# Performance work log

Hardware: AMD Instinct MI355X
Metric: run time of the kernel (lower is better)

The kernel has to match this reference:

```python
import jax, jax.numpy as jnp
import numpy as np

N_HEADS = 16
EPS = 1e-4


def setup_inputs() -> dict:
    key = jax.random.key(0)
    ks = jax.random.split(key, 9)
    B, L, E = 4, 4096, 1024
    s = 1.0 / np.sqrt(E)
    return {
        "x": jax.random.normal(ks[0], (B, L, E), dtype=jnp.float32),
        "Wq": jax.random.normal(ks[1], (E, E), dtype=jnp.float32) * s,
        "bq": jax.random.normal(ks[2], (E,), dtype=jnp.float32) * 0.01,
        "Wk": jax.random.normal(ks[3], (E, E), dtype=jnp.float32) * s,
        "bk": jax.random.normal(ks[4], (E,), dtype=jnp.float32) * 0.01,
        "Wv": jax.random.normal(ks[5], (E, E), dtype=jnp.float32) * s,
        "bv": jax.random.normal(ks[6], (E,), dtype=jnp.float32) * 0.01,
        "Wo": jax.random.normal(ks[7], (E, E), dtype=jnp.float32) * s,
        "bo": jax.random.normal(ks[8], (E,), dtype=jnp.float32) * 0.01,
    }


def _cosformer(x, Wq, bq, Wk, bk, Wv, bv, Wo, bo):
    B, L, E = x.shape
    H = N_HEADS
    hd = E // H
    # torch Linear: y = x @ W.T + b; self-attention so q=k=v source is x
    q = jax.nn.relu(jnp.einsum('ble,fe->blf', x, Wq) + bq)
    k = jax.nn.relu(jnp.einsum('ble,fe->blf', x, Wk) + bk)
    v = jnp.einsum('ble,fe->blf', x, Wv) + bv
    # (B, L, E) -> (B*H, L, hd)  [matches torch view(L, B*H, hd).transpose(0,1)]
    def split_heads(t):
        return t.reshape(B, L, H, hd).transpose(0, 2, 1, 3).reshape(B * H, L, hd)
    q, k, v = split_heads(q), split_heads(k), split_heads(v)
    m = L  # src_len == tgt_len
    idx = (np.pi / 2) * jnp.arange(1, m + 1, dtype=jnp.float32) / m  # (m,)
    sin = jnp.sin(idx)[None, :, None]
    cos = jnp.cos(idx)[None, :, None]
    q_ = jnp.concatenate([q * sin, q * cos], axis=-1)  # (BH, L, 2hd)
    k_ = jnp.concatenate([k * sin, k * cos], axis=-1)
    kv = jnp.einsum('nld,nlm->ndm', k_, v)             # (BH, 2hd, hd)
    z = 1.0 / jnp.maximum(jnp.einsum('nld,nd->nl', q_, k_.sum(axis=1)), EPS)
    attn = jnp.einsum('nld,ndm->nlm', q_, kv) * z[:, :, None]  # (BH, L, hd)
    # (B*H, L, hd) -> (B, L, E)
    out = attn.reshape(B, H, L, hd).transpose(0, 2, 1, 3).reshape(B, L, E)
    return jnp.einsum('ble,fe->blf', out, Wo) + bo


def reference(x, Wq, bq, Wk, bk, Wv, bv, Wo, bo):
    return _cosformer(x, Wq, bq, Wk, bk, Wv, bv, Wo, bo)
```

## Files before the change

kernel.cpp:

```cpp
#include <hip/hip_runtime.h>


typedef unsigned short u16;
typedef unsigned int u32;
typedef __attribute__((ext_vector_type(8))) __bf16 bf16x8;
typedef __attribute__((ext_vector_type(4))) float f32x4;

#define PI_HALF 1.57079632679489662f
#define EPS_Z 1e-4f

__device__ __forceinline__ u16 f32_to_bf16(float f) {
    union { float f; unsigned int u; } x; x.f = f;
    unsigned int lsb = (x.u >> 16) & 1u;
    x.u += 0x7fffu + lsb;
    return (u16)(x.u >> 16);
}
__device__ __forceinline__ float bf16_to_f32(u16 u) {
    union { float f; unsigned int u; } x; x.u = ((unsigned int)u) << 16;
    return x.f;
}

typedef __attribute__((address_space(1))) void amdgpu_global_t;
typedef __attribute__((address_space(3))) void amdgpu_lds_t;
__device__ __forceinline__ void async_load16(const u16* g, u16* l) {
    __builtin_amdgcn_global_load_lds((amdgpu_global_t*)g, (amdgpu_lds_t*)l, 16, 0, 0);
}

__global__ __launch_bounds__(256) void cvt_bf16(const float* __restrict__ in,
                                                u16* __restrict__ out, int n4) {
    int i = blockIdx.x * 256 + threadIdx.x;
    if (i >= n4) return;
    float4 f = ((const float4*)in)[i];
    ushort4 o;
    o.x = f32_to_bf16(f.x); o.y = f32_to_bf16(f.y);
    o.z = f32_to_bf16(f.z); o.w = f32_to_bf16(f.w);
    ((ushort4*)out)[i] = o;
}

__global__ __launch_bounds__(256) void cvt_w4(const float* __restrict__ w0,
                                              const float* __restrict__ w1,
                                              const float* __restrict__ w2,
                                              const float* __restrict__ w3,
                                              u16* __restrict__ wcat) {
    const float* src = (blockIdx.y == 0) ? w0 : (blockIdx.y == 1) ? w1
                     : (blockIdx.y == 2) ? w2 : w3;
    u16* dst = wcat + (size_t)blockIdx.y * 1048576;
    int i = blockIdx.x * 256 + threadIdx.x;
    float4 f = ((const float4*)src)[i];
    ushort4 o;
    o.x = f32_to_bf16(f.x); o.y = f32_to_bf16(f.y);
    o.z = f32_to_bf16(f.z); o.w = f32_to_bf16(f.w);
    ((ushort4*)dst)[i] = o;
}

__global__ __launch_bounds__(256) void gemm_qkv(const u16* __restrict__ A,
                                                const u16* __restrict__ Wcat,
                                                const float* __restrict__ bq,
                                                const float* __restrict__ bk,
                                                const float* __restrict__ bv,
                                                u16* __restrict__ qo,
                                                u16* __restrict__ kTo,
                                                u16* __restrict__ vTo) {
    __shared__ u16 As[128 * 32];
    __shared__ u16 Bs[128 * 32];
    const int K = 1024;
    const int tid  = threadIdx.x;
    const int wave = tid >> 6;
    const int lane = tid & 63;
    const int quad = lane >> 4;
    const int l15  = lane & 15;
    const long tileM = (long)blockIdx.x * 128;
    const long tileN = (long)blockIdx.y * 128;
    const int mat = blockIdx.y >> 3;
    const float* bias = (mat == 0) ? bq : (mat == 1) ? bk : bv;
    const int wm = (wave >> 1) * 64;
    const int wn = (wave & 1) * 64;
    const int s_row = wave * 32 + (lane >> 2);
    const int s_col = (lane & 3) * 8;

    const u16* gA = A    + (tileM + s_row) * (long)K + s_col;
    const u16* gB = Wcat + (tileN + s_row) * (long)K + s_col;
    u16* lA = &As[wave * 1024];
    u16* lB = &Bs[wave * 1024];

    f32x4 acc[4][4] = {};

    for (int kb = 0; kb < K; kb += 32) {
        async_load16(gA,                lA);
        async_load16(gA + 16 * (long)K, lA + 512);
        async_load16(gB,                lB);
        async_load16(gB + 16 * (long)K, lB + 512);
        gA += 32; gB += 32;
        __syncthreads();
        bf16x8 af[4], bf[4];
#pragma unroll
        for (int i = 0; i < 4; i++) {
            af[i] = *(const bf16x8*)&As[(wm + i * 16 + l15) * 32 + quad * 8];
            bf[i] = *(const bf16x8*)&Bs[(wn + i * 16 + l15) * 32 + quad * 8];
        }
#pragma unroll
        for (int i = 0; i < 4; i++)
#pragma unroll
            for (int j = 0; j < 4; j++)
                acc[i][j] = __builtin_amdgcn_mfma_f32_16x16x32_bf16(
                    af[i], bf[j], acc[i][j], 0, 0, 0);
        __syncthreads();
    }

    if (mat == 0) {
#pragma unroll
        for (int j = 0; j < 4; j++) {
            const int nl = (int)(tileN + wn + j * 16 + l15) & 1023;
            const float bv_ = bias[nl];
#pragma unroll
            for (int i = 0; i < 4; i++) {
                const long m0 = tileM + wm + i * 16 + quad * 4;
#pragma unroll
                for (int r = 0; r < 4; r++) {
                    float v = fmaxf(acc[i][j][r] + bv_, 0.0f);
                    qo[(m0 + r) * 1024 + nl] = f32_to_bf16(v);
                }
            }
        }
    } else {
        u16* outT = (mat == 1) ? kTo : vTo;
        const bool relu = (mat == 1);
#pragma unroll
        for (int j = 0; j < 4; j++) {
            const int nl = (int)(tileN + wn + j * 16 + l15) & 1023;
            const float bv_ = bias[nl];
#pragma unroll
            for (int i = 0; i < 4; i++) {
                const long m0 = tileM + wm + i * 16 + quad * 4;
                float v0 = acc[i][j][0] + bv_;
                float v1 = acc[i][j][1] + bv_;
                float v2 = acc[i][j][2] + bv_;
                float v3 = acc[i][j][3] + bv_;
                if (relu) {
                    v0 = fmaxf(v0, 0.0f); v1 = fmaxf(v1, 0.0f);
                    v2 = fmaxf(v2, 0.0f); v3 = fmaxf(v3, 0.0f);
                }
                u32 p0 = (u32)f32_to_bf16(v0) | ((u32)f32_to_bf16(v1) << 16);
                u32 p1 = (u32)f32_to_bf16(v2) | ((u32)f32_to_bf16(v3) << 16);
                u32* dst = (u32*)(outT + (size_t)nl * 16384 + m0);
                dst[0] = p0; dst[1] = p1;
            }
        }
    }
}

__global__ __launch_bounds__(256) void gemm_o(const u16* __restrict__ A,
                                              const u16* __restrict__ Bw,
                                              const float* __restrict__ bias,
                                              float* __restrict__ Cout,
                                              int M, int N, int K) {
    __shared__ u16 As[128 * 32];
    __shared__ u16 Bs[128 * 32];
    const int tid  = threadIdx.x;
    const int wave = tid >> 6;
    const int lane = tid & 63;
    const int quad = lane >> 4;
    const int l15  = lane & 15;
    const long tileM = (long)blockIdx.x * 128;
    const long tileN = (long)blockIdx.y * 128;
    const int wm = (wave >> 1) * 64;
    const int wn = (wave & 1) * 64;
    const int s_row = wave * 32 + (lane >> 2);
    const int s_col = (lane & 3) * 8;

    const u16* gA = A  + (tileM + s_row) * (long)K + s_col;
    const u16* gB = Bw + (tileN + s_row) * (long)K + s_col;
    u16* lA = &As[wave * 1024];
    u16* lB = &Bs[wave * 1024];

    f32x4 acc[4][4] = {};

    for (int kb = 0; kb < K; kb += 32) {
        async_load16(gA,                lA);
        async_load16(gA + 16 * (long)K, lA + 512);
        async_load16(gB,                lB);
        async_load16(gB + 16 * (long)K, lB + 512);
        gA += 32; gB += 32;
        __syncthreads();
        bf16x8 af[4], bf[4];
#pragma unroll
        for (int i = 0; i < 4; i++) {
            af[i] = *(const bf16x8*)&As[(wm + i * 16 + l15) * 32 + quad * 8];
            bf[i] = *(const bf16x8*)&Bs[(wn + i * 16 + l15) * 32 + quad * 8];
        }
#pragma unroll
        for (int i = 0; i < 4; i++)
#pragma unroll
            for (int j = 0; j < 4; j++)
                acc[i][j] = __builtin_amdgcn_mfma_f32_16x16x32_bf16(
                    af[i], bf[j], acc[i][j], 0, 0, 0);
        __syncthreads();
    }

#pragma unroll
    for (int j = 0; j < 4; j++) {
        const long n = tileN + wn + j * 16 + l15;
        const float bv = bias[n];
#pragma unroll
        for (int i = 0; i < 4; i++) {
            const long m0 = tileM + wm + i * 16 + quad * 4;
#pragma unroll
            for (int r = 0; r < 4; r++)
                Cout[(m0 + r) * (long)N + n] = acc[i][j][r] + bv;
        }
    }
}

__global__ __launch_bounds__(256) void kv_mfma(const u16* __restrict__ kT,
                                               const u16* __restrict__ vT,
                                               u16* __restrict__ part) {
    const int tid = threadIdx.x;
    const int wave = tid >> 6, lane = tid & 63;
    const int quad = lane >> 4, l15 = lane & 15;
    const int head = blockIdx.y;
    const int b = head >> 4, h = head & 15;
    const long col0 = (long)b * 4096 + blockIdx.x * 256 + quad * 8;
    const bool use_cos = (wave >> 1) != 0;
    const int mbase = wave * 32;

    const u16* ka[2];
#pragma unroll
    for (int i = 0; i < 2; i++) {
        const int d = (mbase + i * 16 + l15) & 63;
        ka[i] = kT + (size_t)(h * 64 + d) * 16384 + col0;
    }
    const u16* va[4];
#pragma unroll
    for (int j = 0; j < 4; j++) {
        const int n = j * 16 + l15;
        va[j] = vT + (size_t)(h * 64 + n) * 16384 + col0;
    }

    float sv[8], cv[8];
#pragma unroll
    for (int e = 0; e < 8; e++) {
        float ang = (PI_HALF / 4096.0f) * (float)(blockIdx.x * 256 + quad * 8 + e + 1);
        sv[e] = sinf(ang); cv[e] = cosf(ang);
    }
    const float cD = 0.9999247018391445f;
    const float sD = 0.0122715382857199f;

    bf16x8 onesf;
#pragma unroll
    for (int e = 0; e < 8; e++)
        onesf[e] = (l15 == 0) ? (__bf16)1.0f : (__bf16)0.0f;

    f32x4 acc[2][5] = {};

    for (int kt = 0; kt < 8; kt++) {
        bf16x8 kraw[2], bfr[5];
#pragma unroll
        for (int i = 0; i < 2; i++) kraw[i] = *(const bf16x8*)(ka[i] + kt * 32);
#pragma unroll
        for (int j = 0; j < 4; j++) bfr[j] = *(const bf16x8*)(va[j] + kt * 32);
        bfr[4] = onesf;
        bf16x8 af[2];
#pragma unroll
        for (int i = 0; i < 2; i++)
#pragma unroll
            for (int e = 0; e < 8; e++)
                af[i][e] = (__bf16)((float)kraw[i][e] * (use_cos ? cv[e] : sv[e]));
#pragma unroll
        for (int i = 0; i < 2; i++)
#pragma unroll
            for (int j = 0; j < 5; j++)
                acc[i][j] = __builtin_amdgcn_mfma_f32_16x16x32_bf16(
                    af[i], bfr[j], acc[i][j], 0, 0, 0);
#pragma unroll
        for (int e = 0; e < 8; e++) {
            const float ns = sv[e] * cD + cv[e] * sD;
            cv[e] = cv[e] * cD - sv[e] * sD;
            sv[e] = ns;
        }
    }

    u16* op = part + ((size_t)blockIdx.x * 64 + head) * 10240;
#pragma unroll
    for (int i = 0; i < 2; i++)
#pragma unroll
        for (int j = 0; j < 5; j++)
#pragma unroll
            for (int r = 0; r < 4; r++)
                op[(mbase + i * 16 + quad * 4 + r) * 80 + j * 16 + l15] =
                    f32_to_bf16(acc[i][j][r]);
}

__global__ __launch_bounds__(256) void kv_reduce_t(const u16* __restrict__ part,
                                                   u16* __restrict__ Bt) {
    __shared__ float accs[32 * 81];
    const int head = blockIdx.y, d2t = blockIdx.x;
    const u16* bp = part + (size_t)head * 10240 + d2t * 32 * 80;
    for (int idx = threadIdx.x; idx < 2560; idx += 256) {
        float s = 0.0f;
#pragma unroll
        for (int c = 0; c < 16; c++)
            s += bf16_to_f32(bp[(size_t)c * 655360 + idx]);
        const int d2 = idx / 80, n = idx - d2 * 80;
        accs[d2 * 81 + n] = s;
    }
    __syncthreads();
    for (int idx = threadIdx.x; idx < 2560; idx += 256) {
        const int n = idx >> 5, d2 = idx & 31;
        Bt[(size_t)head * 10240 + n * 128 + d2t * 32 + d2] =
            f32_to_bf16(accs[d2 * 81 + n]);
    }
}

__global__ __launch_bounds__(256) void attn_mfma(const u16* __restrict__ qb,
                                                 const u16* __restrict__ Bt,
                                                 u16* __restrict__ merged) {
    __shared__ __align__(16) u16 As[128 * 72];
    __shared__ __align__(16) u16 Bs[80 * 136];
    const int tid = threadIdx.x;
    const int wave = tid >> 6, lane = tid & 63;
    const int quad = lane >> 4, l15 = lane & 15;
    const int head = blockIdx.y;
    const int b = head >> 4, h = head & 15;
    const int tm = blockIdx.x * 128;
    const long b4 = (long)b * 4096;

    for (int c = tid; c < 1024; c += 256) {
        const int row = c >> 3, c8 = c & 7;
        uint4 t = *(const uint4*)(qb + (b4 + tm + row) * 1024 + h * 64 + c8 * 8);
        *(uint4*)&As[row * 72 + c8 * 8] = t;
    }
    for (int c = tid; c < 1280; c += 256) {
        const int row = c >> 4, c16 = c & 15;
        uint4 t = *(const uint4*)(Bt + (long)head * 10240 + row * 128 + c16 * 8);
        *(uint4*)&Bs[row * 136 + c16 * 8] = t;
    }
    const int wm = wave * 32;
    float snl[2], csl[2];
#pragma unroll
    for (int i = 0; i < 2; i++) {
        const int l = tm + wm + i * 16 + l15;
        const float idx = PI_HALF * (float)(l + 1) * (1.0f / 4096.0f);
        snl[i] = sinf(idx); csl[i] = cosf(idx);
    }
    __syncthreads();

    f32x4 acc[2][5] = {};
#pragma unroll
    for (int kb = 0; kb < 4; kb++) {
        const int qc = (kb & 1) * 32 + quad * 8;
        bf16x8 af[2];
#pragma unroll
        for (int i = 0; i < 2; i++) {
            bf16x8 raw = *(const bf16x8*)&As[(wm + i * 16 + l15) * 72 + qc];
            const float s = (kb < 2) ? snl[i] : csl[i];
            bf16x8 sc;
#pragma unroll
            for (int e = 0; e < 8; e++) sc[e] = (__bf16)((float)raw[e] * s);
            af[i] = sc;
        }
        bf16x8 bf[5];
#pragma unroll
        for (int j = 0; j < 5; j++)
            bf[j] = *(const bf16x8*)&Bs[(j * 16 + l15) * 136 + kb * 32 + quad * 8];
#pragma unroll
        for (int i = 0; i < 2; i++)
#pragma unroll
            for (int j = 0; j < 5; j++)
                acc[i][j] = __builtin_amdgcn_mfma_f32_16x16x32_bf16(
                    af[i], bf[j], acc[i][j], 0, 0, 0);
    }

#pragma unroll
    for (int i = 0; i < 2; i++) {
        float z[4];
#pragma unroll
        for (int r = 0; r < 4; r++) {
            const float den = __shfl(acc[i][4][r], lane & 0x30, 64);
            z[r] = 1.0f / fmaxf(den, EPS_Z);
        }
#pragma unroll
        for (int j = 0; j < 4; j++)
#pragma unroll
            for (int r = 0; r < 4; r++) {
                const int l = tm + wm + i * 16 + quad * 4 + r;
                merged[(b4 + l) * 1024 + h * 64 + j * 16 + l15] =
                    f32_to_bf16(acc[i][j][r] * z[r]);
            }
    }
}

extern "C" void kernel_launch(void* const* d_in, const int* in_sizes, int n_in,
                              void* d_out, int out_size, void* d_ws, size_t ws_size,
                              hipStream_t stream) {
    (void)in_sizes; (void)n_in; (void)out_size; (void)ws_size;
    const float* x  = (const float*)d_in[0];
    const float* Wq = (const float*)d_in[1];
    const float* bq = (const float*)d_in[2];
    const float* Wk = (const float*)d_in[3];
    const float* bk = (const float*)d_in[4];
    const float* Wv = (const float*)d_in[5];
    const float* bv = (const float*)d_in[6];
    const float* Wo = (const float*)d_in[7];
    const float* bo = (const float*)d_in[8];
    float* out = (float*)d_out;

    const int M = 16384, E = 1024;
    char* ws = (char*)d_ws;
    const size_t MB = 1048576;
    u16* xb   = (u16*)(ws);
    u16* qb   = (u16*)(ws + 32 * MB);
    u16* kTb  = (u16*)(ws + 64 * MB);
    u16* vTb  = (u16*)(ws + 96 * MB);
    u16* wcat = (u16*)(ws + 128 * MB);
    u16* wob  = wcat + 3 * (size_t)E * E;
    u16* Btb  = (u16*)(ws + 136 * MB);
    u16* partb = xb;
    u16* mergedb = kTb;

    cvt_bf16<<<dim3(M * E / 4 / 256), dim3(256), 0, stream>>>(x, xb, M * E / 4);
    cvt_w4<<<dim3(E * E / 4 / 256, 4), dim3(256), 0, stream>>>(Wq, Wk, Wv, Wo, wcat);

    gemm_qkv<<<dim3(M / 128, 24), dim3(256), 0, stream>>>(xb, wcat, bq, bk, bv,
                                                          qb, kTb, vTb);

    kv_mfma<<<dim3(16, 64), dim3(256), 0, stream>>>(kTb, vTb, partb);
    kv_reduce_t<<<dim3(4, 64), dim3(256), 0, stream>>>(partb, Btb);
    attn_mfma<<<dim3(32, 64), dim3(256), 0, stream>>>(qb, Btb, mergedb);

    gemm_o<<<dim3(M / 128, E / 128), dim3(256), 0, stream>>>(mergedb, wob, bo,
                                                             out, M, E, E);
}
```

Before: 413.5 us.

## Move K/V transpose out of QKV GEMM epilogue; load attention operands directly

The QKV GEMM now writes K and V row-major like Q, with one shared epilogue, instead of scattering transposed 4-byte stores. Two new LDS-tiled transpose kernels then build the K^T and V^T layouts that kv_mfma expects. Workspace buffers are re-aliased so the transposes can reuse freed regions. Separately, attn_mfma drops its LDS staging and barrier and loads Q and the per-head KV matrix straight from global memory into registers. The cost is an extra read and write of K and V plus two more kernel launches.

```diff
diff --git a/kernel.cpp b/kernel.cpp
--- a/kernel.cpp
+++ b/kernel.cpp
@@ -59,8 +59,8 @@
                                                 const float* __restrict__ bk,
                                                 const float* __restrict__ bv,
                                                 u16* __restrict__ qo,
-                                                u16* __restrict__ kTo,
-                                                u16* __restrict__ vTo) {
+                                                u16* __restrict__ ko,
+                                                u16* __restrict__ vo) {
     __shared__ u16 As[128 * 32];
     __shared__ u16 Bs[128 * 32];
     const int K = 1024;
@@ -73,6 +73,8 @@
     const long tileN = (long)blockIdx.y * 128;
     const int mat = blockIdx.y >> 3;
     const float* bias = (mat == 0) ? bq : (mat == 1) ? bk : bv;
+    u16* outp = (mat == 0) ? qo : (mat == 1) ? ko : vo;
+    const bool relu = (mat < 2);
     const int wm = (wave >> 1) * 64;
     const int wn = (wave & 1) * 64;
     const int s_row = wave * 32 + (lane >> 2);
@@ -107,43 +109,18 @@
         __syncthreads();
     }
 
-    if (mat == 0) {
-#pragma unroll
-        for (int j = 0; j < 4; j++) {
-            const int nl = (int)(tileN + wn + j * 16 + l15) & 1023;
-            const float bv_ = bias[nl];
-#pragma unroll
-            for (int i = 0; i < 4; i++) {
-                const long m0 = tileM + wm + i * 16 + quad * 4;
-#pragma unroll
-                for (int r = 0; r < 4; r++) {
-                    float v = fmaxf(acc[i][j][r] + bv_, 0.0f);
-                    qo[(m0 + r) * 1024 + nl] = f32_to_bf16(v);
-                }
-            }
-        }
-    } else {
-        u16* outT = (mat == 1) ? kTo : vTo;
-        const bool relu = (mat == 1);
-#pragma unroll
-        for (int j = 0; j < 4; j++) {
-            const int nl = (int)(tileN + wn + j * 16 + l15) & 1023;
-            const float bv_ = bias[nl];
-#pragma unroll
-            for (int i = 0; i < 4; i++) {
-                const long m0 = tileM + wm + i * 16 + quad * 4;
-                float v0 = acc[i][j][0] + bv_;
-                float v1 = acc[i][j][1] + bv_;
-                float v2 = acc[i][j][2] + bv_;
-                float v3 = acc[i][j][3] + bv_;
-                if (relu) {
-                    v0 = fmaxf(v0, 0.0f); v1 = fmaxf(v1, 0.0f);
-                    v2 = fmaxf(v2, 0.0f); v3 = fmaxf(v3, 0.0f);
-                }
-                u32 p0 = (u32)f32_to_bf16(v0) | ((u32)f32_to_bf16(v1) << 16);
-                u32 p1 = (u32)f32_to_bf16(v2) | ((u32)f32_to_bf16(v3) << 16);
-                u32* dst = (u32*)(outT + (size_t)nl * 16384 + m0);
-                dst[0] = p0; dst[1] = p1;
+#pragma unroll
+    for (int j = 0; j < 4; j++) {
+        const int nl = (int)(tileN + wn + j * 16 + l15) & 1023;
+        const float bv_ = bias[nl];
+#pragma unroll
+        for (int i = 0; i < 4; i++) {
+            const long m0 = tileM + wm + i * 16 + quad * 4;
+#pragma unroll
+            for (int r = 0; r < 4; r++) {
+                float v = acc[i][j][r] + bv_;
+                if (relu) v = fmaxf(v, 0.0f);
+                outp[(m0 + r) * 1024 + nl] = f32_to_bf16(v);
             }
         }
     }
@@ -211,6 +188,33 @@
     }
 }
 
+__global__ __launch_bounds__(256) void transpose_64(const u16* __restrict__ src,
+                                                    u16* __restrict__ dst) {
+    __shared__ u32 tl[64 * 33];
+    const int t = threadIdx.x;
+    const int tok0 = blockIdx.x * 64;
+    const int f0 = blockIdx.y * 64;
+    const int lp = t >> 3;
+    const int d0 = (t & 7) * 8;
+    const u16* s0 = src + (size_t)(tok0 + 2 * lp) * 1024 + f0 + d0;
+    uint4 r0 = *(const uint4*)s0;
+    uint4 r1 = *(const uint4*)(s0 + 1024);
+    const u16* a = (const u16*)&r0;
+    const u16* b_ = (const u16*)&r1;
+#pragma unroll
+    for (int e = 0; e < 8; e++)
+        tl[(d0 + e) * 33 + lp] = (u32)a[e] | ((u32)b_[e] << 16);
+    __syncthreads();
+    const int d = t >> 2;
+    const int lg = (t & 3) * 8;
+    u32 o[8];
+#pragma unroll
+    for (int e = 0; e < 8; e++) o[e] = tl[d * 33 + lg + e];
+    u16* dp = dst + (size_t)(f0 + d) * 16384 + tok0 + lg * 2;
+    *(uint4*)(dp)     = *(const uint4*)&o[0];
+    *(uint4*)(dp + 8) = *(const uint4*)&o[4];
+}
+
 __global__ __launch_bounds__(256) void kv_mfma(const u16* __restrict__ kT,
                                                const u16* __restrict__ vT,
                                                u16* __restrict__ part) {
@@ -314,8 +318,6 @@
 __global__ __launch_bounds__(256) void attn_mfma(const u16* __restrict__ qb,
                                                  const u16* __restrict__ Bt,
                                                  u16* __restrict__ merged) {
-    __shared__ __align__(16) u16 As[128 * 72];
-    __shared__ __align__(16) u16 Bs[80 * 136];
     const int tid = threadIdx.x;
     const int wave = tid >> 6, lane = tid & 63;
     const int quad = lane >> 4, l15 = lane & 15;
@@ -323,18 +325,16 @@
     const int b = head >> 4, h = head & 15;
     const int tm = blockIdx.x * 128;
     const long b4 = (long)b * 4096;
-
-    for (int c = tid; c < 1024; c += 256) {
-        const int row = c >> 3, c8 = c & 7;
-        uint4 t = *(const uint4*)(qb + (b4 + tm + row) * 1024 + h * 64 + c8 * 8);
-        *(uint4*)&As[row * 72 + c8 * 8] = t;
-    }
-    for (int c = tid; c < 1280; c += 256) {
-        const int row = c >> 4, c16 = c & 15;
-        uint4 t = *(const uint4*)(Bt + (long)head * 10240 + row * 128 + c16 * 8);
-        *(uint4*)&Bs[row * 136 + c16 * 8] = t;
-    }
     const int wm = wave * 32;
+
+    bf16x8 q0[2], q1[2];
+#pragma unroll
+    for (int i = 0; i < 2; i++) {
+        const u16* qp = qb + (size_t)(b4 + tm + wm + i * 16 + l15) * 1024
+                      + h * 64 + quad * 8;
+        q0[i] = *(const bf16x8*)qp;
+        q1[i] = *(const bf16x8*)(qp + 32);
+    }
     float snl[2], csl[2];
 #pragma unroll
     for (int i = 0; i < 2; i++) {
@@ -342,32 +342,29 @@
         const float idx = PI_HALF * (float)(l + 1) * (1.0f / 4096.0f);
         snl[i] = sinf(idx); csl[i] = cosf(idx);
     }
-    __syncthreads();
-
+
+    const u16* bp = Bt + (size_t)head * 10240 + quad * 8;
     f32x4 acc[2][5] = {};
 #pragma unroll
     for (int kb = 0; kb < 4; kb++) {
-        const int qc = (kb & 1) * 32 + quad * 8;
+        bf16x8 bfr[5];
+#pragma unroll
+        for (int j = 0; j < 5; j++)
+            bfr[j] = *(const bf16x8*)(bp + (size_t)(j * 16 + l15) * 128 + kb * 32);
         bf16x8 af[2];
 #pragma unroll
         for (int i = 0; i < 2; i++) {
-            bf16x8 raw = *(const bf16x8*)&As[(wm + i * 16 + l15) * 72 + qc];
+            bf16x8 raw = (kb & 1) ? q1[i] : q0[i];
             const float s = (kb < 2) ? snl[i] : csl[i];
-            bf16x8 sc;
-#pragma unroll
-            for (int e = 0; e < 8; e++) sc[e] = (__bf16)((float)raw[e] * s);
-            af[i] = sc;
-        }
-        bf16x8 bf[5];
-#pragma unroll
-        for (int j = 0; j < 5; j++)
-            bf[j] = *(const bf16x8*)&Bs[(j * 16 + l15) * 136 + kb * 32 + quad * 8];
+#pragma unroll
+            for (int e = 0; e < 8; e++) af[i][e] = (__bf16)((float)raw[e] * s);
+        }
 #pragma unroll
         for (int i = 0; i < 2; i++)
 #pragma unroll
             for (int j = 0; j < 5; j++)
                 acc[i][j] = __builtin_amdgcn_mfma_f32_16x16x32_bf16(
-                    af[i], bf[j], acc[i][j], 0, 0, 0);
+                    af[i], bfr[j], acc[i][j], 0, 0, 0);
     }
 
 #pragma unroll
@@ -409,19 +406,24 @@
     const size_t MB = 1048576;
     u16* xb   = (u16*)(ws);
     u16* qb   = (u16*)(ws + 32 * MB);
-    u16* kTb  = (u16*)(ws + 64 * MB);
-    u16* vTb  = (u16*)(ws + 96 * MB);
+    u16* kb   = (u16*)(ws + 64 * MB);
+    u16* vb   = (u16*)(ws + 96 * MB);
     u16* wcat = (u16*)(ws + 128 * MB);
     u16* wob  = wcat + 3 * (size_t)E * E;
     u16* Btb  = (u16*)(ws + 136 * MB);
-    u16* partb = xb;
-    u16* mergedb = kTb;
+    u16* kTb  = xb;
+    u16* vTb  = kb;
+    u16* partb = vb;
+    u16* mergedb = kb;
 
     cvt_bf16<<<dim3(M * E / 4 / 256), dim3(256), 0, stream>>>(x, xb, M * E / 4);
     cvt_w4<<<dim3(E * E / 4 / 256, 4), dim3(256), 0, stream>>>(Wq, Wk, Wv, Wo, wcat);
 
     gemm_qkv<<<dim3(M / 128, 24), dim3(256), 0, stream>>>(xb, wcat, bq, bk, bv,
-                                                          qb, kTb, vTb);
+                                                          qb, kb, vb);
+
+    transpose_64<<<dim3(256, 16), dim3(256), 0, stream>>>(kb, kTb);
+    transpose_64<<<dim3(256, 16), dim3(256), 0, stream>>>(vb, vTb);
 
     kv_mfma<<<dim3(16, 64), dim3(256), 0, stream>>>(kTb, vTb, partb);
     kv_reduce_t<<<dim3(4, 64), dim3(256), 0, stream>>>(partb, Btb);
```

Result: slower. 422.0 us (+2.1%).
